# Optimization experiments

Hardware: AMD Instinct MI355X
Metric: run time of the kernel (lower is better)

Reference implementation:

```python
import jax, jax.numpy as jnp
import numpy as np

B, S, D, E, H, K = 2, 2048, 1024, 8, 2048, 2
EM_ITERS = 5
LB_WEIGHT = 0.1
EPS = 1e-8


def setup_inputs() -> dict:
    key = jax.random.key(0)
    ks = jax.random.split(key, 12)
    sc = 0.02
    return {
        "x": jax.random.normal(ks[0], (B, S, D), jnp.float32),
        "gate_W": jax.random.normal(ks[1], (D, E), jnp.float32) * sc,
        "gate_b": jnp.zeros((E,), jnp.float32),
        "gate_temp": jnp.ones((1,), jnp.float32),
        "W1": jax.random.normal(ks[2], (E, D, H), jnp.float32) * sc,
        "b1": jnp.zeros((E, H), jnp.float32),
        "W2": jax.random.normal(ks[3], (E, H, D), jnp.float32) * sc,
        "b2": jnp.zeros((E, D), jnp.float32),
        "sW1": jax.random.normal(ks[4], (D, H), jnp.float32) * sc,
        "sb1": jnp.zeros((H,), jnp.float32),
        "sW2": jax.random.normal(ks[5], (H, D), jnp.float32) * sc,
        "sb2": jnp.zeros((D,), jnp.float32),
    }


def reference(x, gate_W, gate_b, gate_temp, W1, b1, W2, b2, sW1, sb1, sW2, sb2):
    Bq, Sq, Dq = x.shape
    T = Bq * Sq
    xf = x.reshape(T, Dq)  # (T, D)

    # Router: gate linear + learned temperature
    gate_logits = xf @ gate_W + gate_b              # (T, E)
    tempered = gate_logits / gate_temp               # (T, E)
    expert_weights = jax.nn.softmax(tempered, axis=-1)
    _, topk_idx = jax.lax.top_k(expert_weights, K)   # (T, K) int32
    first = topk_idx[:, 0]

    # Load-balance loss: KL(uniform || empirical top-1 usage) (fresh counters)
    usage = jnp.zeros((E,), jnp.float32).at[first].add(1.0)
    actual = usage / jnp.float32(T)
    actual = actual + EPS
    actual = actual / actual.sum()
    u = jnp.float32(1.0 / E)
    kl = jnp.sum(u * (jnp.log(u) - jnp.log(actual)))
    load_balance_loss = LB_WEIGHT * kl

    # EM expert-load reweighting on tempered logits
    scores = jax.nn.softmax(tempered, axis=-1)       # (T, E)
    p = jnp.full((E,), 1.0 / E, jnp.float32)
    for _ in range(EM_ITERS):
        ea = scores * p                               # (T, E)
        ea = ea / (ea.sum(axis=-1, keepdims=True) + EPS)
        counts = ea.sum(axis=0)                       # (E,)
        p = counts / (counts.sum() + EPS)
    balanced = scores * p                             # (T, E)

    # All-expert FFN (dense, equivalent to per-expert masked compute)
    h = jax.nn.relu(jnp.einsum('td,edh->teh', xf, W1) + b1)  # (T, E, H)
    eo = jnp.einsum('teh,ehd->ted', h, W2) + b2              # (T, E, D)

    # Combine top-k experts with balanced weights
    w_k = jnp.take_along_axis(balanced, topk_idx, axis=1)        # (T, K)
    out_k = jnp.take_along_axis(eo, topk_idx[:, :, None], axis=1)  # (T, K, D)
    out = jnp.einsum('tk,tkd->td', w_k, out_k)                   # (T, D)

    # Shared expert, weighted by 0.1
    shared = jax.nn.relu(xf @ sW1 + sb1) @ sW2 + sb2
    out = out + 0.1 * shared

    return out.reshape(Bq, Sq, Dq), load_balance_loss
```

## Files before the change

### kernel.cpp

```cpp
#include <hip/hip_runtime.h>
#include <math.h>

#define T_TOK 4096
#define D_DIM 1024
#define H_DIM 2048
#define NE 8
#define EPSF 1e-8f
#define G1_GEMM 448
#define G2_GEMM 224
#define NTR128 1152

typedef __attribute__((ext_vector_type(8))) short bf16x8;
typedef __attribute__((ext_vector_type(4))) float f32x4;

__device__ __forceinline__ unsigned short f2bf(float f) {
  unsigned u = __float_as_uint(f);
  u += 0x7fffu + ((u >> 16) & 1u);
  return (unsigned short)(u >> 16);
}

__device__ __forceinline__ float bf2f(unsigned short u) {
  return __uint_as_float((unsigned)u << 16);
}

__device__ __forceinline__ void gload_lds16(const void* g, void* l) {
  __builtin_amdgcn_global_load_lds(
      (const __attribute__((address_space(1))) unsigned int*)g,
      (__attribute__((address_space(3))) unsigned int*)l, 16, 0, 0);
}

#define WAITV(n) asm volatile("s_waitcnt vmcnt(" #n ")" ::: "memory")
#define BARR()                                  \
  do {                                          \
    asm volatile("" ::: "memory");              \
    __builtin_amdgcn_s_barrier();               \
    asm volatile("" ::: "memory");              \
  } while (0)

__device__ __forceinline__ void transpose_tile128(const float* __restrict__ src,
                                                  unsigned short* __restrict__ dst,
                                                  int R, int C, int r0, int c0, int tid,
                                                  float* tile) {
#pragma unroll
  for (int k = 0; k < 8; ++k) {
    int id = tid + k * 512;
    int row = id >> 5, c4 = (id & 31) * 4;
    float4 v = *(const float4*)(src + (size_t)(r0 + row) * C + c0 + c4);
    float* tr = tile + row * 129 + c4;
    tr[0] = v.x; tr[1] = v.y; tr[2] = v.z; tr[3] = v.w;
  }
  __syncthreads();
#pragma unroll
  for (int k = 0; k < 4; ++k) {
    int id = tid + k * 512;
    int oc = id >> 4;
    int rbase = (id & 15) * 8;
    uint4 wv;
    unsigned* wp = (unsigned*)&wv;
#pragma unroll
    for (int j = 0; j < 4; ++j) {
      unsigned lo = f2bf(tile[(rbase + 2 * j) * 129 + oc]);
      unsigned hi = f2bf(tile[(rbase + 2 * j + 1) * 129 + oc]);
      wp[j] = lo | (hi << 16);
    }
    *(uint4*)(dst + (size_t)(c0 + oc) * R + r0 + rbase) = wv;
  }
}

__global__ __launch_bounds__(512, 4) void prep2_kernel(
    const float* __restrict__ x, const float* __restrict__ gW, const float* __restrict__ gb,
    const float* __restrict__ gtemp, const float* __restrict__ W1, const float* __restrict__ sW1,
    unsigned short* __restrict__ W1t, unsigned short* __restrict__ sW1t,
    unsigned short* __restrict__ xb, float* __restrict__ scores, int* __restrict__ idx,
    unsigned* __restrict__ usage, unsigned* __restrict__ cnt, int* __restrict__ perm) {
  __shared__ char psm[67584];
  int b = blockIdx.x, tid = threadIdx.x;
  if (b >= 512) {
    int l = b - 512;
    int m = l >> 7, rem = l & 127;
    int c0 = (rem & 15) * 128, r0 = (rem >> 4) * 128;
    const float* src = (m < NE) ? W1 + (size_t)m * D_DIM * H_DIM : sW1;
    unsigned short* dst = (m < NE) ? W1t + (size_t)m * D_DIM * H_DIM : sW1t;
    transpose_tile128(src, dst, D_DIM, H_DIM, r0, c0, tid, (float*)psm);
    return;
  }
  float* gWl = (float*)psm;
  int* toks = (int*)(psm + 36864);
  int wave = tid >> 6, lane = tid & 63;
  int t0 = b * 8;
#pragma unroll
  for (int k = 0; k < 4; ++k) {
    int q = tid + k * 512;
    float4 f = ((const float4*)gW)[q];
    int d = q >> 1, eo = (q & 1) * 4;
    float* dstv = &gWl[d * 9 + eo];
    dstv[0] = f.x; dstv[1] = f.y; dstv[2] = f.z; dstv[3] = f.w;
  }
  __syncthreads();
  int t = t0 + wave;
  const float* xr = x + (size_t)t * D_DIM;
  unsigned short* xbr = xb + (size_t)t * D_DIM;
  float part[NE];
#pragma unroll
  for (int e = 0; e < NE; ++e) part[e] = 0.f;
#pragma unroll
  for (int i = 0; i < 16; ++i) {
    int d = lane + 64 * i;
    float xv = xr[d];
    xbr[d] = f2bf(xv);
    const float* g = &gWl[d * 9];
#pragma unroll
    for (int e = 0; e < NE; ++e) part[e] += xv * g[e];
  }
#pragma unroll
  for (int e = 0; e < NE; ++e) {
    float v = part[e];
    for (int off = 32; off; off >>= 1) v += __shfl_xor(v, off);
    part[e] = v;
  }
  float temp = gtemp[0];
  float mx = -1e30f;
#pragma unroll
  for (int e = 0; e < NE; ++e) { part[e] = (part[e] + gb[e]) / temp; mx = fmaxf(mx, part[e]); }
  float s = 0.f;
#pragma unroll
  for (int e = 0; e < NE; ++e) { part[e] = expf(part[e] - mx); s += part[e]; }
  float inv = 1.0f / s;
#pragma unroll
  for (int e = 0; e < NE; ++e) part[e] *= inv;
  if (lane == 0) {
    float4* sp = (float4*)(scores + (size_t)t * NE);
    sp[0] = make_float4(part[0], part[1], part[2], part[3]);
    sp[1] = make_float4(part[4], part[5], part[6], part[7]);
    int i0 = 0; float b0 = part[0];
#pragma unroll
    for (int e = 1; e < NE; ++e) if (part[e] > b0) { b0 = part[e]; i0 = e; }
    int i1 = -1; float b1 = -1e30f;
#pragma unroll
    for (int e = 0; e < NE; ++e) if (e != i0 && part[e] > b1) { b1 = part[e]; i1 = e; }
    idx[t * 2] = i0; idx[t * 2 + 1] = i1;
    toks[wave * 2] = i0; toks[wave * 2 + 1] = i1;
  }
  __syncthreads();
  if (tid < NE) {
    int c0 = 0, c1 = 0;
#pragma unroll
    for (int j = 0; j < 8; ++j) {
      if (toks[j * 2] == tid) ++c0;
      if (toks[j * 2 + 1] == tid) ++c1;
    }
    if (c0) atomicAdd(&usage[tid], (unsigned)c0);
    int tot = c0 + c1;
    if (tot) {
      unsigned bb = atomicAdd(&cnt[tid], (unsigned)tot);
      int p = 0;
#pragma unroll
      for (int j = 0; j < 8; ++j) {
        if (toks[j * 2] == tid) perm[(size_t)tid * T_TOK + bb + p++] = (t0 + j) * 2;
        if (toks[j * 2 + 1] == tid) perm[(size_t)tid * T_TOK + bb + p++] = (t0 + j) * 2 + 1;
      }
    }
  }
}

__device__ __forceinline__ void em_block512(const float* __restrict__ scores,
                                            const unsigned* __restrict__ usage,
                                            float* __restrict__ p_out, float* __restrict__ loss_out,
                                            int tid, char* smem) {
  float* p_sh = (float*)smem;
  float* cw = p_sh + 8;
  float* counts_sh = cw + 64;
  int wave = tid >> 6, lane = tid & 63;
  float s[8][NE];
#pragma unroll
  for (int rr = 0; rr < 8; ++rr) {
    int row = tid + rr * 512;
    const float4* sp = (const float4*)(scores + (size_t)row * NE);
    float4 a = sp[0], b = sp[1];
    s[rr][0] = a.x; s[rr][1] = a.y; s[rr][2] = a.z; s[rr][3] = a.w;
    s[rr][4] = b.x; s[rr][5] = b.y; s[rr][6] = b.z; s[rr][7] = b.w;
  }
  if (tid < NE) p_sh[tid] = 1.0f / NE;
  __syncthreads();
  for (int it = 0; it < 5; ++it) {
    float p[NE];
#pragma unroll
    for (int e = 0; e < NE; ++e) p[e] = p_sh[e];
    float c[NE];
#pragma unroll
    for (int e = 0; e < NE; ++e) c[e] = 0.f;
#pragma unroll
    for (int rr = 0; rr < 8; ++rr) {
      float denom = 0.f;
#pragma unroll
      for (int e = 0; e < NE; ++e) denom += s[rr][e] * p[e];
      float inv = 1.0f / (denom + EPSF);
#pragma unroll
      for (int e = 0; e < NE; ++e) c[e] += s[rr][e] * p[e] * inv;
    }
#pragma unroll
    for (int e = 0; e < NE; ++e) {
      float v = c[e];
      for (int off = 32; off; off >>= 1) v += __shfl_xor(v, off);
      c[e] = v;
    }
    if (lane == 0) {
#pragma unroll
      for (int e = 0; e < NE; ++e) cw[wave * 8 + e] = c[e];
    }
    __syncthreads();
    if (tid < NE) {
      float tot = 0.f;
#pragma unroll
      for (int w = 0; w < 8; ++w) tot += cw[w * 8 + tid];
      counts_sh[tid] = tot;
    }
    __syncthreads();
    if (tid < NE) {
      float total = 0.f;
#pragma unroll
      for (int e = 0; e < NE; ++e) total += counts_sh[e];
      p_sh[tid] = counts_sh[tid] / (total + EPSF);
    }
    __syncthreads();
  }
  if (tid < NE) p_out[tid] = p_sh[tid];
  if (tid == 0) {
    float actual[NE]; float norm = 0.f;
#pragma unroll
    for (int e = 0; e < NE; ++e) { actual[e] = (float)usage[e] / (float)T_TOK + EPSF; norm += actual[e]; }
    float u = 1.0f / NE;
    float kl = 0.f;
#pragma unroll
    for (int e = 0; e < NE; ++e) kl += u * (logf(u) - logf(actual[e] / norm));
    loss_out[0] = 0.1f * kl;
  }
}

template <int KDIM, int NDIM, bool RELU, bool MODE1, bool OBF16>
__device__ __forceinline__ void gemm_body(
    unsigned short* lds, int flat,
    const unsigned short* __restrict__ A, const unsigned short* __restrict__ WE,
    const unsigned short* __restrict__ WS, const float* __restrict__ biasE,
    const float* __restrict__ biasS, const int* __restrict__ perm,
    const unsigned* __restrict__ cnt, void* __restrict__ outp) {
  constexpr int BM = 256, BN = 256, BK = 64;
  constexpr int NT = NDIM / BN;
  constexpr int NKT = KDIM / BK;

  int tc[9];
#pragma unroll
  for (int i = 0; i < NE; ++i) tc[i] = ((int)cnt[i] + 255) >> 8;
  tc[8] = T_TOK / 256;
  int nt = 0;
#pragma unroll
  for (int i = 0; i < 9; ++i) nt += tc[i];
  int W = nt * NT;
  int xcd = flat & 7, pos = flat >> 3;
  int q = W >> 3, r = W & 7;
  int mycount = q + (xcd < r ? 1 : 0);
  if (pos >= mycount) return;
  int mystart = xcd * q + (xcd < r ? xcd : r);
  int w = mystart + pos;
  int ti = w / NT;
  int n0 = (w % NT) * BN;
  int e = 0, mt = ti;
  while (mt >= tc[e]) { mt -= tc[e]; ++e; }
  int m0 = mt * BM;
  int cnt_e = (e == NE) ? T_TOK : (int)cnt[e];

  const unsigned short* Bmat = (e == NE) ? WS : WE + (size_t)e * KDIM * NDIM;
  const float* bias = (e == NE) ? biasS : biasE + (size_t)e * NDIM;

  int tid = threadIdx.x, wave = tid >> 6, lane = tid & 63;
  int wm = wave >> 1, wn = wave & 1;
  int frow = lane & 15, fks = lane >> 4;

  int srow = wave * 8 + (lane >> 3);
  int sslot = lane & 7;
  const unsigned short* aptr[2][2];
  const unsigned short* bptr[2][2];
#pragma unroll
  for (int h = 0; h < 2; ++h)
#pragma unroll
    for (int j = 0; j < 2; ++j) {
      int rr = h * 128 + j * 64 + srow;
      int colsw = (sslot ^ (rr & 7)) << 3;
      int ar = m0 + rr;
      if (ar > cnt_e - 1) ar = cnt_e - 1;
      int gar;
      if (e == NE) gar = MODE1 ? ar : (2 * T_TOK + ar);
      else { int v = perm[(size_t)e * T_TOK + ar]; gar = MODE1 ? (v >> 1) : v; }
      aptr[h][j] = A + (size_t)gar * KDIM + colsw;
      bptr[h][j] = Bmat + (size_t)(n0 + rr) * KDIM + colsw;
    }

  auto stA = [&](int t, int h) {
    int dbe = (t & 1) * 16384;
    int k0 = t * BK;
    gload_lds16(aptr[h][0] + k0, &lds[dbe + h * 8192 + wave * 512]);
    gload_lds16(aptr[h][1] + k0, &lds[dbe + h * 8192 + wave * 512 + 4096]);
  };
  auto stB = [&](int t, int h) {
    int dbe = (t & 1) * 16384;
    int k0 = t * BK;
    gload_lds16(bptr[h][0] + k0, &lds[32768 + dbe + h * 8192 + wave * 512]);
    gload_lds16(bptr[h][1] + k0, &lds[32768 + dbe + h * 8192 + wave * 512 + 4096]);
  };

  auto rdA = [&](int dbe, int ks, int m) -> bf16x8 {
    int rr = wm * 64 + m * 16 + frow;
    int slot = (ks * 4 + fks) ^ (rr & 7);
    return *(const bf16x8*)&lds[dbe + rr * 64 + slot * 8];
  };
  auto rdB = [&](int dbe, int ks, int bh, int jj) -> bf16x8 {
    int rr = bh * 128 + jj * 32 + wn * 16 + frow;
    int slot = (ks * 4 + fks) ^ (rr & 7);
    return *(const bf16x8*)&lds[32768 + dbe + rr * 64 + slot * 8];
  };

  f32x4 acc[4][8];
#pragma unroll
  for (int m = 0; m < 4; ++m)
#pragma unroll
    for (int nn = 0; nn < 8; ++nn) acc[m][nn] = (f32x4){0.f, 0.f, 0.f, 0.f};

  stA(0, 0); stA(0, 1);
  stB(0, 0); stB(0, 1);
  stA(1, 0); stA(1, 1);
  WAITV(4);
  BARR();

  for (int t = 0; t < NKT; ++t) {
    const int dbe = (t & 1) * 16384;
    bf16x8 a0[4], a1[4], b0[4], b1[4];

#pragma unroll
    for (int m = 0; m < 4; ++m) a0[m] = rdA(dbe, 0, m);
#pragma unroll
    for (int m = 0; m < 4; ++m) a1[m] = rdA(dbe, 1, m);
#pragma unroll
    for (int jj = 0; jj < 4; ++jj) b0[jj] = rdB(dbe, 0, 0, jj);
#pragma unroll
    for (int jj = 0; jj < 4; ++jj) b1[jj] = rdB(dbe, 1, 0, jj);
    if (t + 1 < NKT) { stB(t + 1, 0); stB(t + 1, 1); }
    BARR();
    __builtin_amdgcn_s_setprio(1);
#pragma unroll
    for (int m = 0; m < 4; ++m)
#pragma unroll
      for (int jj = 0; jj < 4; ++jj)
        acc[m][jj] = __builtin_amdgcn_mfma_f32_16x16x32_bf16(a0[m], b0[jj], acc[m][jj], 0, 0, 0);
#pragma unroll
    for (int m = 0; m < 4; ++m)
#pragma unroll
      for (int jj = 0; jj < 4; ++jj)
        acc[m][jj] = __builtin_amdgcn_mfma_f32_16x16x32_bf16(a1[m], b1[jj], acc[m][jj], 0, 0, 0);
    __builtin_amdgcn_s_setprio(0);
    BARR();

#pragma unroll
    for (int jj = 0; jj < 4; ++jj) b0[jj] = rdB(dbe, 0, 1, jj);
#pragma unroll
    for (int jj = 0; jj < 4; ++jj) b1[jj] = rdB(dbe, 1, 1, jj);
    if (t + 2 < NKT) { stA(t + 2, 0); stA(t + 2, 1); }
    BARR();
    __builtin_amdgcn_s_setprio(1);
#pragma unroll
    for (int m = 0; m < 4; ++m)
#pragma unroll
      for (int jj = 0; jj < 4; ++jj)
        acc[m][4 + jj] = __builtin_amdgcn_mfma_f32_16x16x32_bf16(a0[m], b0[jj], acc[m][4 + jj], 0, 0, 0);
#pragma unroll
    for (int m = 0; m < 4; ++m)
#pragma unroll
      for (int jj = 0; jj < 4; ++jj)
        acc[m][4 + jj] = __builtin_amdgcn_mfma_f32_16x16x32_bf16(a1[m], b1[jj], acc[m][4 + jj], 0, 0, 0);
    __builtin_amdgcn_s_setprio(0);
    if (t + 2 < NKT) { WAITV(4); }
    else if (t + 1 < NKT) { WAITV(0); }
    BARR();
  }

#pragma unroll
  for (int m = 0; m < 4; ++m) {
#pragma unroll
    for (int qq = 0; qq < 4; ++qq) {
      int rt = wm * 64 + m * 16 + (lane >> 4) * 4 + qq;
      if (m0 + rt >= cnt_e) continue;
      int rr;
      if (e == NE) rr = 2 * T_TOK + m0 + rt;
      else rr = perm[(size_t)e * T_TOK + m0 + rt];
#pragma unroll
      for (int nn = 0; nn < 8; ++nn) {
        int col = n0 + (nn >> 2) * 128 + (nn & 3) * 32 + wn * 16 + (lane & 15);
        float val = acc[m][nn][qq] + bias[col];
        if (RELU) val = fmaxf(val, 0.f);
        if (MODE1 || OBF16)
          ((unsigned short*)outp)[(size_t)rr * NDIM + col] = f2bf(val);
        else
          ((float*)outp)[(size_t)rr * NDIM + col] = val;
      }
    }
  }
}

__global__ __launch_bounds__(512, 2) void gemm1_kernel(
    const unsigned short* __restrict__ xb, const unsigned short* __restrict__ W1t,
    const unsigned short* __restrict__ sW1t, const float* __restrict__ b1,
    const float* __restrict__ sb1, const int* __restrict__ perm, const unsigned* __restrict__ cnt,
    unsigned short* __restrict__ Hbuf,
    const float* __restrict__ W2, const float* __restrict__ sW2,
    unsigned short* __restrict__ W2t, unsigned short* __restrict__ sW2t,
    const float* __restrict__ scores, const unsigned* __restrict__ usage,
    float* __restrict__ pbuf, float* __restrict__ loss_out) {
  __shared__ char smem[131072];
  int flat = blockIdx.x;
  if (flat < G1_GEMM) {
    gemm_body<D_DIM, H_DIM, true, true, false>((unsigned short*)smem, flat, xb, W1t, sW1t, b1,
                                               sb1, perm, cnt, (void*)Hbuf);
    return;
  }
  int l = flat - G1_GEMM;
  if (l < NTR128) {
    int m = l >> 7, rem = l & 127;
    int c0 = (rem & 7) * 128, r0 = (rem >> 3) * 128;
    const float* src = (m < NE) ? W2 + (size_t)m * H_DIM * D_DIM : sW2;
    unsigned short* dst = (m < NE) ? W2t + (size_t)m * H_DIM * D_DIM : sW2t;
    transpose_tile128(src, dst, H_DIM, D_DIM, r0, c0, threadIdx.x, (float*)smem);
    return;
  }
  em_block512(scores, usage, pbuf, loss_out, threadIdx.x, smem);
}

template <int KDIM, int NDIM, bool RELU, bool MODE1, bool OBF16>
__global__ __launch_bounds__(512, 2) void gemm_kernel(
    const unsigned short* __restrict__ A, const unsigned short* __restrict__ WE,
    const unsigned short* __restrict__ WS, const float* __restrict__ biasE,
    const float* __restrict__ biasS, const int* __restrict__ perm,
    const unsigned* __restrict__ cnt, void* __restrict__ outp) {
  __shared__ char smem[131072];
  gemm_body<KDIM, NDIM, RELU, MODE1, OBF16>((unsigned short*)smem, blockIdx.x, A, WE, WS, biasE,
                                            biasS, perm, cnt, outp);
}

__global__ void combine_kernel(const unsigned short* __restrict__ ebuf,
                               const float* __restrict__ scores,
                               const float* __restrict__ p, const int* __restrict__ idx,
                               float* __restrict__ out) {
  int gid = blockIdx.x * blockDim.x + threadIdx.x;
  int t = gid >> 8;
  int d4 = gid & 255;
  int e0 = idx[t * 2], e1 = idx[t * 2 + 1];
  float w0 = scores[(size_t)t * NE + e0] * p[e0];
  float w1 = scores[(size_t)t * NE + e1] * p[e1];
  const ushort4* r0 = (const ushort4*)(ebuf + (size_t)(t * 2) * D_DIM);
  const ushort4* r1 = (const ushort4*)(ebuf + (size_t)(t * 2 + 1) * D_DIM);
  const ushort4* rs = (const ushort4*)(ebuf + (size_t)(2 * T_TOK + t) * D_DIM);
  ushort4 a = r0[d4], b = r1[d4], c = rs[d4];
  float4 o;
  o.x = w0 * bf2f(a.x) + w1 * bf2f(b.x) + 0.1f * bf2f(c.x);
  o.y = w0 * bf2f(a.y) + w1 * bf2f(b.y) + 0.1f * bf2f(c.y);
  o.z = w0 * bf2f(a.z) + w1 * bf2f(b.z) + 0.1f * bf2f(c.z);
  o.w = w0 * bf2f(a.w) + w1 * bf2f(b.w) + 0.1f * bf2f(c.w);
  ((float4*)out)[gid] = o;
}

extern "C" void kernel_launch(void* const* d_in, const int* in_sizes, int n_in,
                              void* d_out, int out_size, void* d_ws, size_t ws_size,
                              hipStream_t stream) {
  const float* x     = (const float*)d_in[0];
  const float* gW    = (const float*)d_in[1];
  const float* gb    = (const float*)d_in[2];
  const float* gtemp = (const float*)d_in[3];
  const float* W1    = (const float*)d_in[4];
  const float* b1    = (const float*)d_in[5];
  const float* W2    = (const float*)d_in[6];
  const float* b2    = (const float*)d_in[7];
  const float* sW1   = (const float*)d_in[8];
  const float* sb1   = (const float*)d_in[9];
  const float* sW2   = (const float*)d_in[10];
  const float* sb2   = (const float*)d_in[11];
  float* out = (float*)d_out;

  char* ws = (char*)d_ws;
  size_t off = 0;
  auto take = [&](size_t b) { char* ptr = ws + off; off += (b + 255) & ~(size_t)255; return ptr; };
  unsigned short* xb   = (unsigned short*)take((size_t)T_TOK * D_DIM * 2);
  unsigned short* W1t  = (unsigned short*)take((size_t)NE * H_DIM * D_DIM * 2);
  unsigned short* sW1t = (unsigned short*)take((size_t)H_DIM * D_DIM * 2);
  unsigned short* W2t  = (unsigned short*)take((size_t)NE * D_DIM * H_DIM * 2);
  unsigned short* sW2t = (unsigned short*)take((size_t)D_DIM * H_DIM * 2);
  unsigned short* Hbuf = (unsigned short*)take((size_t)3 * T_TOK * H_DIM * 2);
  unsigned short* ebuf = (unsigned short*)take((size_t)3 * T_TOK * D_DIM * 2);
  float* scores        = (float*)take((size_t)T_TOK * NE * 4);
  int* idx             = (int*)take((size_t)T_TOK * 2 * 4);
  int* perm            = (int*)take((size_t)NE * T_TOK * 4);
  unsigned* cnt        = (unsigned*)take(256);
  unsigned* usage      = (unsigned*)take(256);
  float* pbuf          = (float*)take(256);
  (void)n_in; (void)in_sizes; (void)out_size; (void)ws_size;

  hipMemsetAsync(cnt, 0, 512, stream);
  prep2_kernel<<<512 + NTR128, 512, 0, stream>>>(x, gW, gb, gtemp, W1, sW1, W1t, sW1t, xb,
                                                 scores, idx, usage, cnt, perm);
  gemm1_kernel<<<G1_GEMM + NTR128 + 1, 512, 0, stream>>>(
      xb, W1t, sW1t, b1, sb1, perm, cnt, Hbuf, W2, sW2, W2t, sW2t, scores, usage, pbuf,
      out + (size_t)T_TOK * D_DIM);
  gemm_kernel<H_DIM, D_DIM, false, false, true><<<G2_GEMM, 512, 0, stream>>>(
      Hbuf, W2t, sW2t, b2, sb2, perm, cnt, (void*)ebuf);
  combine_kernel<<<(T_TOK * D_DIM / 4) / 256, 256, 0, stream>>>(ebuf, scores, pbuf, idx, out);
}
```

Baseline: 191.9 us.

## Split-K the second expert GEMM into two halves summed in combine

The second FFN GEMM (K=2048, N=1024) gets a split-K of two via blockIdx.y. Each half writes its bf16 partial output to a separate buffer, and only the first half adds the bias. The combine kernel reads both partials and sums them before weighting. This doubles the block count of a GEMM with few tiles, which should fill the GPU better. In exchange it adds an extra partial-output buffer to write and read, and an additional bf16 rounding of each partial.

```diff
diff --git a/kernel.cpp b/kernel.cpp
--- a/kernel.cpp
+++ b/kernel.cpp
@@ -237,16 +237,16 @@
   }
 }
 
-template <int KDIM, int NDIM, bool RELU, bool MODE1, bool OBF16>
+template <int STR, int KLEN, int NDIM, bool RELU, bool MODE1, bool OBF16>
 __device__ __forceinline__ void gemm_body(
-    unsigned short* lds, int flat,
+    unsigned short* lds, int flat, int koff,
     const unsigned short* __restrict__ A, const unsigned short* __restrict__ WE,
     const unsigned short* __restrict__ WS, const float* __restrict__ biasE,
     const float* __restrict__ biasS, const int* __restrict__ perm,
     const unsigned* __restrict__ cnt, void* __restrict__ outp) {
   constexpr int BM = 256, BN = 256, BK = 64;
   constexpr int NT = NDIM / BN;
-  constexpr int NKT = KDIM / BK;
+  constexpr int NKT = KLEN / BK;
 
   int tc[9];
 #pragma unroll
@@ -269,8 +269,9 @@
   int m0 = mt * BM;
   int cnt_e = (e == NE) ? T_TOK : (int)cnt[e];
 
-  const unsigned short* Bmat = (e == NE) ? WS : WE + (size_t)e * KDIM * NDIM;
-  const float* bias = (e == NE) ? biasS : biasE + (size_t)e * NDIM;
+  const unsigned short* Bmat = (e == NE) ? WS : WE + (size_t)e * STR * NDIM;
+  const float* biasEx = (e == NE) ? biasS : (biasE ? biasE + (size_t)e * NDIM : nullptr);
+  const float* bias = biasE ? biasEx : nullptr;
 
   int tid = threadIdx.x, wave = tid >> 6, lane = tid & 63;
   int wm = wave >> 1, wn = wave & 1;
@@ -291,8 +292,8 @@
       int gar;
       if (e == NE) gar = MODE1 ? ar : (2 * T_TOK + ar);
       else { int v = perm[(size_t)e * T_TOK + ar]; gar = MODE1 ? (v >> 1) : v; }
-      aptr[h][j] = A + (size_t)gar * KDIM + colsw;
-      bptr[h][j] = Bmat + (size_t)(n0 + rr) * KDIM + colsw;
+      aptr[h][j] = A + (size_t)gar * STR + koff + colsw;
+      bptr[h][j] = Bmat + (size_t)(n0 + rr) * STR + koff + colsw;
     }
 
   auto stA = [&](int t, int h) {
@@ -394,7 +395,7 @@
 #pragma unroll
       for (int nn = 0; nn < 8; ++nn) {
         int col = n0 + (nn >> 2) * 128 + (nn & 3) * 32 + wn * 16 + (lane & 15);
-        float val = acc[m][nn][qq] + bias[col];
+        float val = acc[m][nn][qq] + (bias ? bias[col] : 0.f);
         if (RELU) val = fmaxf(val, 0.f);
         if (MODE1 || OBF16)
           ((unsigned short*)outp)[(size_t)rr * NDIM + col] = f2bf(val);
@@ -417,8 +418,8 @@
   __shared__ char smem[131072];
   int flat = blockIdx.x;
   if (flat < G1_GEMM) {
-    gemm_body<D_DIM, H_DIM, true, true, false>((unsigned short*)smem, flat, xb, W1t, sW1t, b1,
-                                               sb1, perm, cnt, (void*)Hbuf);
+    gemm_body<D_DIM, D_DIM, H_DIM, true, true, false>((unsigned short*)smem, flat, 0, xb, W1t,
+                                                      sW1t, b1, sb1, perm, cnt, (void*)Hbuf);
     return;
   }
   int l = flat - G1_GEMM;
@@ -433,18 +434,24 @@
   em_block512(scores, usage, pbuf, loss_out, threadIdx.x, smem);
 }
 
-template <int KDIM, int NDIM, bool RELU, bool MODE1, bool OBF16>
-__global__ __launch_bounds__(512, 2) void gemm_kernel(
-    const unsigned short* __restrict__ A, const unsigned short* __restrict__ WE,
-    const unsigned short* __restrict__ WS, const float* __restrict__ biasE,
-    const float* __restrict__ biasS, const int* __restrict__ perm,
-    const unsigned* __restrict__ cnt, void* __restrict__ outp) {
+__global__ __launch_bounds__(512, 2) void gemm2_kernel(
+    const unsigned short* __restrict__ Hbuf, const unsigned short* __restrict__ W2t,
+    const unsigned short* __restrict__ sW2t, const float* __restrict__ b2,
+    const float* __restrict__ sb2, const int* __restrict__ perm,
+    const unsigned* __restrict__ cnt, unsigned short* __restrict__ eA,
+    unsigned short* __restrict__ eB) {
   __shared__ char smem[131072];
-  gemm_body<KDIM, NDIM, RELU, MODE1, OBF16>((unsigned short*)smem, blockIdx.x, A, WE, WS, biasE,
-                                            biasS, perm, cnt, outp);
-}
-
-__global__ void combine_kernel(const unsigned short* __restrict__ ebuf,
+  int ks = blockIdx.y;
+  const float* be = ks ? nullptr : b2;
+  const float* bs = ks ? nullptr : sb2;
+  unsigned short* outp = ks ? eB : eA;
+  gemm_body<H_DIM, 1024, D_DIM, false, false, true>((unsigned short*)smem, blockIdx.x, ks * 1024,
+                                                    Hbuf, W2t, sW2t, be, bs, perm, cnt,
+                                                    (void*)outp);
+}
+
+__global__ void combine_kernel(const unsigned short* __restrict__ eA,
+                               const unsigned short* __restrict__ eB,
                                const float* __restrict__ scores,
                                const float* __restrict__ p, const int* __restrict__ idx,
                                float* __restrict__ out) {
@@ -454,15 +461,19 @@
   int e0 = idx[t * 2], e1 = idx[t * 2 + 1];
   float w0 = scores[(size_t)t * NE + e0] * p[e0];
   float w1 = scores[(size_t)t * NE + e1] * p[e1];
-  const ushort4* r0 = (const ushort4*)(ebuf + (size_t)(t * 2) * D_DIM);
-  const ushort4* r1 = (const ushort4*)(ebuf + (size_t)(t * 2 + 1) * D_DIM);
-  const ushort4* rs = (const ushort4*)(ebuf + (size_t)(2 * T_TOK + t) * D_DIM);
-  ushort4 a = r0[d4], b = r1[d4], c = rs[d4];
+  size_t r0 = (size_t)(t * 2) * 256 + d4;
+  size_t r1 = (size_t)(t * 2 + 1) * 256 + d4;
+  size_t rs = (size_t)(2 * T_TOK + t) * 256 + d4;
+  const ushort4* A4 = (const ushort4*)eA;
+  const ushort4* B4 = (const ushort4*)eB;
+  ushort4 a0 = A4[r0], c0 = B4[r0];
+  ushort4 a1 = A4[r1], c1 = B4[r1];
+  ushort4 as = A4[rs], cs = B4[rs];
   float4 o;
-  o.x = w0 * bf2f(a.x) + w1 * bf2f(b.x) + 0.1f * bf2f(c.x);
-  o.y = w0 * bf2f(a.y) + w1 * bf2f(b.y) + 0.1f * bf2f(c.y);
-  o.z = w0 * bf2f(a.z) + w1 * bf2f(b.z) + 0.1f * bf2f(c.z);
-  o.w = w0 * bf2f(a.w) + w1 * bf2f(b.w) + 0.1f * bf2f(c.w);
+  o.x = w0 * (bf2f(a0.x) + bf2f(c0.x)) + w1 * (bf2f(a1.x) + bf2f(c1.x)) + 0.1f * (bf2f(as.x) + bf2f(cs.x));
+  o.y = w0 * (bf2f(a0.y) + bf2f(c0.y)) + w1 * (bf2f(a1.y) + bf2f(c1.y)) + 0.1f * (bf2f(as.y) + bf2f(cs.y));
+  o.z = w0 * (bf2f(a0.z) + bf2f(c0.z)) + w1 * (bf2f(a1.z) + bf2f(c1.z)) + 0.1f * (bf2f(as.z) + bf2f(cs.z));
+  o.w = w0 * (bf2f(a0.w) + bf2f(c0.w)) + w1 * (bf2f(a1.w) + bf2f(c1.w)) + 0.1f * (bf2f(as.w) + bf2f(cs.w));
   ((float4*)out)[gid] = o;
 }
 
@@ -492,7 +503,8 @@
   unsigned short* W2t  = (unsigned short*)take((size_t)NE * D_DIM * H_DIM * 2);
   unsigned short* sW2t = (unsigned short*)take((size_t)D_DIM * H_DIM * 2);
   unsigned short* Hbuf = (unsigned short*)take((size_t)3 * T_TOK * H_DIM * 2);
-  unsigned short* ebuf = (unsigned short*)take((size_t)3 * T_TOK * D_DIM * 2);
+  unsigned short* eA   = (unsigned short*)take((size_t)3 * T_TOK * D_DIM * 2);
+  unsigned short* eB   = (unsigned short*)take((size_t)3 * T_TOK * D_DIM * 2);
   float* scores        = (float*)take((size_t)T_TOK * NE * 4);
   int* idx             = (int*)take((size_t)T_TOK * 2 * 4);
   int* perm            = (int*)take((size_t)NE * T_TOK * 4);
@@ -507,7 +519,6 @@
   gemm1_kernel<<<G1_GEMM + NTR128 + 1, 512, 0, stream>>>(
       xb, W1t, sW1t, b1, sb1, perm, cnt, Hbuf, W2, sW2, W2t, sW2t, scores, usage, pbuf,
       out + (size_t)T_TOK * D_DIM);
-  gemm_kernel<H_DIM, D_DIM, false, false, true><<<G2_GEMM, 512, 0, stream>>>(
-      Hbuf, W2t, sW2t, b2, sb2, perm, cnt, (void*)ebuf);
-  combine_kernel<<<(T_TOK * D_DIM / 4) / 256, 256, 0, stream>>>(ebuf, scores, pbuf, idx, out);
-}
+  gemm2_kernel<<<dim3(G2_GEMM, 2), 512, 0, stream>>>(Hbuf, W2t, sW2t, b2, sb2, perm, cnt, eA, eB);
+  combine_kernel<<<(T_TOK * D_DIM / 4) / 256, 256, 0, stream>>>(eA, eB, scores, pbuf, idx, out);
+}
```

New measurement: 245.1 us. +27.7%, slower.
